# Kernel tuning notes

Hardware: AMD Instinct MI355X
Metric: run time of the kernel (lower is better)

Reference implementation:

```python
import jax, jax.numpy as jnp
import numpy as np

N_NODES = 50000
N_EDGES = 800000


def setup_inputs() -> dict:
    key = jax.random.key(0)
    ks = jax.random.split(key, 9)
    d, h, hd = 128, 4, 32
    s = 1.0 / np.sqrt(d)
    return {
        "x": jax.random.normal(ks[0], (N_NODES, d), jnp.float32),
        "edge_index": jax.random.randint(ks[1], (2, N_EDGES), 0, N_NODES, jnp.int32),
        "W0": jax.random.normal(ks[2], (d, d), jnp.float32) * s,
        "att_l0": jax.random.normal(ks[3], (h, hd), jnp.float32) * s,
        "att_r0": jax.random.normal(ks[4], (h, hd), jnp.float32) * s,
        "b0": jnp.zeros((d,), jnp.float32),
        "W1": jax.random.normal(ks[5], (d, d), jnp.float32) * s,
        "att_l1": jax.random.normal(ks[6], (h, hd), jnp.float32) * s,
        "att_r1": jax.random.normal(ks[7], (h, hd), jnp.float32) * s,
        "b1": jnp.zeros((hd,), jnp.float32),
    }


def _gat_layer(x, src, dst, W, att_l, att_r, bias, concat):
    # x: [N, F_in]; W: [H*D, F_in] (torch Linear layout); att_*: [H, D]
    n = x.shape[0]
    h, d = att_l.shape
    hx = (x @ W.T).reshape(n, h, d)                     # [N,H,D]
    al = jnp.einsum('nhd,hd->nh', hx, att_l)            # [N,H]
    ar = jnp.einsum('nhd,hd->nh', hx, att_r)
    att = al[src] + ar[dst]                             # [E,H]
    att = jax.nn.leaky_relu(att, negative_slope=0.2)
    # segment softmax over destination nodes
    m = jax.ops.segment_max(att, dst, num_segments=n)   # [N,H]
    att = jnp.exp(att - m[dst])
    ssum = jax.ops.segment_sum(att, dst, num_segments=n)
    att = att / (ssum[dst] + 1e-9)                      # [E,H]
    msgs = att[:, :, None] * hx[src]                    # [E,H,D]
    out = jax.ops.segment_sum(msgs, dst, num_segments=n)  # [N,H,D]
    if concat:
        out = out.reshape(n, h * d)
    else:
        out = out.mean(axis=1)
    return out + bias


def reference(x, edge_index, W0, att_l0, att_r0, b0, W1, att_l1, att_r1, b1):
    src, dst = edge_index[0], edge_index[1]
    x = _gat_layer(x, src, dst, W0, att_l0, att_r0, b0, concat=True)
    x = jax.nn.relu(x)  # dropout is identity in eval mode
    x = _gat_layer(x, src, dst, W1, att_l1, att_r1, b1, concat=False)
    return x
```

## Files before the change

### kernel.cpp

```cpp
#include <hip/hip_runtime.h>
#include <hip/hip_bf16.h>

#define H 4
#define D 32
#define F 128
#define MAXDEG 64
#define PF 16
#define NBUCK 256
#define BUCKW 196
#define NABLK 128
#define SEGCAP 64
#define GB    1563
#define HXP   136

typedef __attribute__((ext_vector_type(8))) short bf16x8;
typedef __attribute__((ext_vector_type(4))) float f32x4;

__device__ __forceinline__ short f2bf(float v) {
    __hip_bfloat16 h = __float2bfloat16(v);
    return *reinterpret_cast<short*>(&h);
}
__device__ __forceinline__ float bf2f(short s) {
    __hip_bfloat16 h = *reinterpret_cast<__hip_bfloat16*>(&s);
    return __bfloat162float(h);
}

__device__ __forceinline__
void wconv_part(int part8, const float* __restrict__ W0, short* __restrict__ W0hi,
                short* __restrict__ W0lo, const float* __restrict__ W1,
                short* __restrict__ W1hi, short* __restrict__ W1lo) {
    const int tid = threadIdx.x;
    const float* W  = (part8 < 4) ? W0 : W1;
    short* Whi = (part8 < 4) ? W0hi : W1hi;
    short* Wlo = (part8 < 4) ? W0lo : W1lo;
    const int part = part8 & 3;
    const int base = part * (F * F / 4);
    for (int i = base + tid * 4; i < base + F * F / 4; i += 1024) {
        float4 v = *reinterpret_cast<const float4*>(W + i);
        float vv[4] = {v.x, v.y, v.z, v.w};
        short hs[4], ls[4];
#pragma unroll
        for (int j = 0; j < 4; ++j) {
            hs[j] = f2bf(vv[j]);
            ls[j] = f2bf(vv[j] - bf2f(hs[j]));
        }
        *reinterpret_cast<short4*>(Whi + i) = make_short4(hs[0], hs[1], hs[2], hs[3]);
        *reinterpret_cast<short4*>(Wlo + i) = make_short4(ls[0], ls[1], ls[2], ls[3]);
    }
}

__device__ __forceinline__
void bucketA_body(int abid, const int* __restrict__ ei, int E,
                  int* __restrict__ cntmat, unsigned int* __restrict__ buf) {
    __shared__ int lcnt[NBUCK];
    const int tid = threadIdx.x;
    lcnt[tid] = 0;
    __syncthreads();
    const int per = ((E / NABLK) + 3) & ~3;
    const int e0 = abid * per;
    const int e1 = min(e0 + per, E);
    for (int e = e0 + 4 * tid; e < e1; e += 1024) {
        int4 dv = *reinterpret_cast<const int4*>(ei + E + e);
        atomicAdd(&lcnt[dv.x / BUCKW], 1);
        atomicAdd(&lcnt[dv.y / BUCKW], 1);
        atomicAdd(&lcnt[dv.z / BUCKW], 1);
        atomicAdd(&lcnt[dv.w / BUCKW], 1);
    }
    __syncthreads();
    cntmat[abid * NBUCK + tid] = min(lcnt[tid], SEGCAP);
    lcnt[tid] = 0;
    __syncthreads();
    for (int e = e0 + 4 * tid; e < e1; e += 1024) {
        int4 sv = *reinterpret_cast<const int4*>(ei + e);
        int4 dv = *reinterpret_cast<const int4*>(ei + E + e);
        int ss[4] = {sv.x, sv.y, sv.z, sv.w};
        int dd[4] = {dv.x, dv.y, dv.z, dv.w};
#pragma unroll
        for (int j = 0; j < 4; ++j) {
            int b = dd[j] / BUCKW;
            int pos = atomicAdd(&lcnt[b], 1);
            if (pos < SEGCAP)
                buf[((size_t)b * NABLK + abid) * SEGCAP + pos] =
                    (unsigned)ss[j] | ((unsigned)(dd[j] - b * BUCKW) << 16);
        }
    }
}

__global__ __launch_bounds__(256)
void k_init(const int* __restrict__ ei, int E, int* __restrict__ cntmat,
            unsigned int* __restrict__ buf,
            const float* __restrict__ W0, short* __restrict__ W0hi,
            short* __restrict__ W0lo, const float* __restrict__ W1,
            short* __restrict__ W1hi, short* __restrict__ W1lo) {
    const int bid = blockIdx.x;
    if (bid < NABLK)
        bucketA_body(bid, ei, E, cntmat, buf);
    else
        wconv_part(bid - NABLK, W0, W0hi, W0lo, W1, W1hi, W1lo);
}

__device__ __forceinline__
void bucketB_body(int b, const unsigned int* __restrict__ buf,
                  const int* __restrict__ cntmat, int* __restrict__ deg,
                  unsigned short* __restrict__ ssrc2u, int N,
                  int* cnt, int* scnt, unsigned short* slots) {
    const int tid = threadIdx.x;
    if (tid < BUCKW) cnt[tid] = 0;
    if (tid < NABLK) scnt[tid] = cntmat[tid * NBUCK + b];
    __syncthreads();
    const int a    = tid & (NABLK - 1);
    const int half = tid >> 7;
    const int mm   = scnt[a];
    const unsigned int* seg = buf + ((size_t)b * NABLK + a) * SEGCAP;
    for (int c = half * 4; c < mm; c += 8) {
        uint4 r = *reinterpret_cast<const uint4*>(seg + c);
        unsigned rr[4] = {r.x, r.y, r.z, r.w};
#pragma unroll
        for (int j = 0; j < 4; ++j) {
            if (c + j < mm) {
                int src  = rr[j] & 0xffff;
                int ldst = rr[j] >> 16;
                int slot = atomicAdd(&cnt[ldst], 1);
                if (slot < MAXDEG)
                    slots[ldst * MAXDEG + slot] = (unsigned short)src;
            }
        }
    }
    __syncthreads();
    uint4* dst = reinterpret_cast<uint4*>(ssrc2u + (size_t)b * BUCKW * MAXDEG);
    const uint4* s4 = reinterpret_cast<const uint4*>(slots);
    for (int i = tid; i < BUCKW * MAXDEG / 8; i += 256)
        dst[i] = s4[i];
    if (tid < BUCKW) {
        int node = b * BUCKW + tid;
        if (node < N) deg[node] = cnt[tid];
    }
}

__device__ __forceinline__
void bsetup_pre(const short* __restrict__ Whi, const short* __restrict__ Wlo,
                int wave, int m, int q8, bf16x8 Bhi[2][4], bf16x8 Blo[2][4]) {
#pragma unroll
    for (int j = 0; j < 2; ++j) {
        const int fout = wave * 32 + j * 16 + m;
#pragma unroll
        for (int kc = 0; kc < 4; ++kc) {
            Bhi[j][kc] = *reinterpret_cast<const bf16x8*>(Whi + (size_t)fout * F + kc * 32 + q8);
            Blo[j][kc] = *reinterpret_cast<const bf16x8*>(Wlo + (size_t)fout * F + kc * 32 + q8);
        }
    }
}

__device__ __forceinline__
void loadA_f32(const float* __restrict__ X, int node0, int m, int q8, float4 r[8]) {
    const float* xp = X + (size_t)(node0 + m) * F + q8;
#pragma unroll
    for (int kc = 0; kc < 4; ++kc) {
        r[2 * kc]     = *reinterpret_cast<const float4*>(xp + kc * 32);
        r[2 * kc + 1] = *reinterpret_cast<const float4*>(xp + kc * 32 + 4);
    }
}

__device__ __forceinline__
void splitA(const float4 r[8], bf16x8 Ahi[4], bf16x8 Alo[4]) {
#pragma unroll
    for (int kc = 0; kc < 4; ++kc) {
        float xv[8] = {r[2 * kc].x, r[2 * kc].y, r[2 * kc].z, r[2 * kc].w,
                       r[2 * kc + 1].x, r[2 * kc + 1].y, r[2 * kc + 1].z, r[2 * kc + 1].w};
#pragma unroll
        for (int t2 = 0; t2 < 8; ++t2) {
            short hh = f2bf(xv[t2]);
            Ahi[kc][t2] = hh;
            Alo[kc][t2] = f2bf(xv[t2] - bf2f(hh));
        }
    }
}

__device__ __forceinline__
void mfma_epi(int tile, const bf16x8 Ahi[4], const bf16x8 Alo[4],
              const bf16x8 Bhi[2][4], const bf16x8 Blo[2][4],
              float alw0, float alw16, float arw0, float arw16,
              short* hxs, float* __restrict__ AL,
              float* __restrict__ AR, int wave, int m, int q) {
    const int node0 = tile * 16;
    f32x4 acc0 = {0.f, 0.f, 0.f, 0.f};
    f32x4 acc1 = {0.f, 0.f, 0.f, 0.f};
#pragma unroll
    for (int kc = 0; kc < 4; ++kc) {
        acc0 = __builtin_amdgcn_mfma_f32_16x16x32_bf16(Ahi[kc], Bhi[0][kc], acc0, 0, 0, 0);
        acc1 = __builtin_amdgcn_mfma_f32_16x16x32_bf16(Ahi[kc], Bhi[1][kc], acc1, 0, 0, 0);
        acc0 = __builtin_amdgcn_mfma_f32_16x16x32_bf16(Ahi[kc], Blo[0][kc], acc0, 0, 0, 0);
        acc1 = __builtin_amdgcn_mfma_f32_16x16x32_bf16(Ahi[kc], Blo[1][kc], acc1, 0, 0, 0);
        acc0 = __builtin_amdgcn_mfma_f32_16x16x32_bf16(Alo[kc], Bhi[0][kc], acc0, 0, 0, 0);
        acc1 = __builtin_amdgcn_mfma_f32_16x16x32_bf16(Alo[kc], Bhi[1][kc], acc1, 0, 0, 0);
    }
    const int row0 = node0 + q * 4;
    const int col0 = wave * 32 + m;
#pragma unroll
    for (int r = 0; r < 4; ++r) {
        hxs[(q * 4 + r) * HXP + col0]      = f2bf(acc0[r]);
        hxs[(q * 4 + r) * HXP + col0 + 16] = f2bf(acc1[r]);
        float pal = acc0[r] * alw0 + acc1[r] * alw16;
        float par = acc0[r] * arw0 + acc1[r] * arw16;
#pragma unroll
        for (int o = 1; o < 16; o <<= 1) {
            pal += __shfl_xor(pal, o);
            par += __shfl_xor(par, o);
        }
        if (m == 0) {
            AL[(size_t)(row0 + r) * H + wave] = pal;
            AR[(size_t)(row0 + r) * H + wave] = par;
        }
    }
}

__device__ __forceinline__
void hxb_writeout(const short* hxs, int tile, __hip_bfloat16* __restrict__ HXB) {
    const int tid = threadIdx.x;
    const int row = tid >> 4;
    const int col = (tid & 15) * 8;
    uint4 v = *reinterpret_cast<const uint4*>(hxs + row * HXP + col);
    *reinterpret_cast<uint4*>(reinterpret_cast<short*>(HXB) +
                              (size_t)(tile * 16 + row) * F + col) = v;
}

__device__ __forceinline__
void gemm_pair_f32(int bid, const float* __restrict__ X,
                   const short* __restrict__ Whi, const short* __restrict__ Wlo,
                   const float* __restrict__ attl, const float* __restrict__ attr,
                   __hip_bfloat16* __restrict__ HXB, float* __restrict__ AL,
                   float* __restrict__ AR, int ntiles, short* hxs) {
    const int wave = threadIdx.x >> 6;
    const int lane = threadIdx.x & 63;
    const int m    = lane & 15;
    const int q    = lane >> 4;
    const int q8   = q * 8;
    bf16x8 Bhi[2][4], Blo[2][4];
    bsetup_pre(Whi, Wlo, wave, m, q8, Bhi, Blo);
    const float alw0  = attl[wave * 32 + m];
    const float alw16 = attl[wave * 32 + 16 + m];
    const float arw0  = attr[wave * 32 + m];
    const float arw16 = attr[wave * 32 + 16 + m];

    const int t0 = bid, t1 = bid + GB;
    const bool has1 = t1 < ntiles;
    float4 r0[8], r1[8];
    loadA_f32(X, t0 * 16, m, q8, r0);
    if (has1) loadA_f32(X, t1 * 16, m, q8, r1);
    bf16x8 Ahi[4], Alo[4];
    splitA(r0, Ahi, Alo);
    mfma_epi(t0, Ahi, Alo, Bhi, Blo, alw0, alw16, arw0, arw16, hxs, AL, AR, wave, m, q);
    if (has1) {
        splitA(r1, Ahi, Alo);
        mfma_epi(t1, Ahi, Alo, Bhi, Blo, alw0, alw16, arw0, arw16,
                 hxs + 16 * HXP, AL, AR, wave, m, q);
    }
    __syncthreads();
    hxb_writeout(hxs, t0, HXB);
    if (has1) hxb_writeout(hxs + 16 * HXP, t1, HXB);
}

__global__ __launch_bounds__(256)
void k_mid(const unsigned int* __restrict__ buf, const int* __restrict__ cntmat,
           int* __restrict__ deg, unsigned short* __restrict__ ssrc2u, int N,
           const float* __restrict__ X, const short* __restrict__ W0hi,
           const short* __restrict__ W0lo, const float* __restrict__ attl0,
           const float* __restrict__ attr0, __hip_bfloat16* __restrict__ HXB,
           float* __restrict__ AL, float* __restrict__ AR, int ntiles) {
    __shared__ union {
        struct {
            int cnt[BUCKW];
            int scnt[NABLK];
            unsigned short slots[BUCKW * MAXDEG];
        } bb;
        short hxs[2 * 16 * HXP];
    } sm;
    const int bid = blockIdx.x;
    if (bid < NBUCK)
        bucketB_body(bid, buf, cntmat, deg, ssrc2u, N,
                     sm.bb.cnt, sm.bb.scnt, sm.bb.slots);
    else
        gemm_pair_f32(bid - NBUCK, X, W0hi, W0lo, attl0, attr0, HXB, AL, AR,
                      ntiles, sm.hxs);
}

__device__ __forceinline__
int stage_node32(int g2, int lt, int n, const unsigned short* __restrict__ ssrc2u,
                 const int* __restrict__ deg, const float* __restrict__ AL,
                 const float4 ar4, int (*sidx)[MAXDEG], float (*sw)[MAXDEG][H]) {
    const int cnt  = min(deg[n], MAXDEG);
    const int rcnt = (cnt + PF - 1) & ~(PF - 1);
    for (int t2 = lt; t2 < rcnt; t2 += 32) {
        if (t2 < cnt) {
            int s = ssrc2u[(size_t)n * MAXDEG + t2];
            sidx[g2][t2] = s;
            float4 al4 = *reinterpret_cast<const float4*>(AL + (size_t)s * H);
            float a0 = al4.x + ar4.x; a0 = a0 > 0.f ? a0 : 0.2f * a0;
            float a1 = al4.y + ar4.y; a1 = a1 > 0.f ? a1 : 0.2f * a1;
            float a2 = al4.z + ar4.z; a2 = a2 > 0.f ? a2 : 0.2f * a2;
            float a3 = al4.w + ar4.w; a3 = a3 > 0.f ? a3 : 0.2f * a3;
            sw[g2][t2][0] = __expf(a0);
            sw[g2][t2][1] = __expf(a1);
            sw[g2][t2][2] = __expf(a2);
            sw[g2][t2][3] = __expf(a3);
        } else {
            sidx[g2][t2] = 0;
            sw[g2][t2][0] = 0.f; sw[g2][t2][1] = 0.f;
            sw[g2][t2][2] = 0.f; sw[g2][t2][3] = 0.f;
        }
    }
    __builtin_amdgcn_wave_barrier();
    return rcnt;
}

__device__ __forceinline__
void gather32(int g2, int lt, int rcnt, const __hip_bfloat16* __restrict__ HXB,
              const int (*sidx)[MAXDEG], const float (*sw)[MAXDEG][H],
              float& a0, float& a1, float& a2, float& a3, float& wsum) {
    const int h = lt >> 3;
    const unsigned short* hx = reinterpret_cast<const unsigned short*>(HXB);
    for (int base = 0; base < rcnt; base += PF) {
        ushort4 v[PF];
#pragma unroll
        for (int j = 0; j < PF; ++j) {
            int s = sidx[g2][base + j];
            v[j] = *reinterpret_cast<const ushort4*>(hx + (size_t)s * F + 4 * lt);
        }
#pragma unroll
        for (int j = 0; j < PF; ++j) {
            float w = sw[g2][base + j][h];
            a0 += w * bf2f((short)v[j].x);
            a1 += w * bf2f((short)v[j].y);
            a2 += w * bf2f((short)v[j].z);
            a3 += w * bf2f((short)v[j].w);
            wsum += w;
        }
    }
}

__global__ __launch_bounds__(256)
void k_ag1(const unsigned short* __restrict__ ssrc2u, const int* __restrict__ deg,
           const float* __restrict__ AL0, const float* __restrict__ AR0,
           const __hip_bfloat16* __restrict__ HXB0, const float* __restrict__ b0,
           const short* __restrict__ W1hi, const short* __restrict__ W1lo,
           const float* __restrict__ attl1, const float* __restrict__ attr1,
           __hip_bfloat16* __restrict__ HXB1, float* __restrict__ AL1,
           float* __restrict__ AR1, int ntiles) {
    __shared__ int   sidx[8][MAXDEG];
    __shared__ float sw[8][MAXDEG][H];
    __shared__ short x1h[16 * HXP];
    __shared__ short x1l[16 * HXP];
    const int tid  = threadIdx.x;
    const int g2   = tid >> 5;
    const int lt   = tid & 31;
    const int tile = blockIdx.x;

#pragma unroll
    for (int r = 0; r < 2; ++r) {
        const int n = tile * 16 + r * 8 + g2;
        const float4 ar4 = *reinterpret_cast<const float4*>(AR0 + (size_t)n * H);
        int rcnt = stage_node32(g2, lt, n, ssrc2u, deg, AL0, ar4, sidx, sw);
        float a0 = 0.f, a1 = 0.f, a2 = 0.f, a3 = 0.f, ws = 0.f;
        gather32(g2, lt, rcnt, HXB0, sidx, sw, a0, a1, a2, a3, ws);
        float inv = 1.f / (ws + 1e-9f);
        const float4 b4 = *reinterpret_cast<const float4*>(b0 + 4 * lt);
        float o0 = fmaxf(a0 * inv + b4.x, 0.f);
        float o1 = fmaxf(a1 * inv + b4.y, 0.f);
        float o2 = fmaxf(a2 * inv + b4.z, 0.f);
        float o3 = fmaxf(a3 * inv + b4.w, 0.f);
        short h0 = f2bf(o0), h1 = f2bf(o1), h2 = f2bf(o2), h3 = f2bf(o3);
        short l0 = f2bf(o0 - bf2f(h0)), l1 = f2bf(o1 - bf2f(h1));
        short l2 = f2bf(o2 - bf2f(h2)), l3 = f2bf(o3 - bf2f(h3));
        const int row = r * 8 + g2;
        uint2 hw, lw;
        hw.x = (unsigned)(unsigned short)h0 | ((unsigned)(unsigned short)h1 << 16);
        hw.y = (unsigned)(unsigned short)h2 | ((unsigned)(unsigned short)h3 << 16);
        lw.x = (unsigned)(unsigned short)l0 | ((unsigned)(unsigned short)l1 << 16);
        lw.y = (unsigned)(unsigned short)l2 | ((unsigned)(unsigned short)l3 << 16);
        *reinterpret_cast<uint2*>(x1h + row * HXP + 4 * lt) = hw;
        *reinterpret_cast<uint2*>(x1l + row * HXP + 4 * lt) = lw;
    }
    __syncthreads();

    short* hxs = reinterpret_cast<short*>(sw);
    {
        const int wave = tid >> 6;
        const int lane = tid & 63;
        const int m    = lane & 15;
        const int q    = lane >> 4;
        const int q8   = q * 8;
        bf16x8 Bhi[2][4], Blo[2][4];
        bsetup_pre(W1hi, W1lo, wave, m, q8, Bhi, Blo);
        const float alw0  = attl1[wave * 32 + m];
        const float alw16 = attl1[wave * 32 + 16 + m];
        const float arw0  = attr1[wave * 32 + m];
        const float arw16 = attr1[wave * 32 + 16 + m];
        bf16x8 Ahi[4], Alo[4];
#pragma unroll
        for (int kc = 0; kc < 4; ++kc) {
            Ahi[kc] = *reinterpret_cast<const bf16x8*>(x1h + m * HXP + kc * 32 + q8);
            Alo[kc] = *reinterpret_cast<const bf16x8*>(x1l + m * HXP + kc * 32 + q8);
        }
        mfma_epi(tile, Ahi, Alo, Bhi, Blo, alw0, alw16, arw0, arw16,
                 hxs, AL1, AR1, wave, m, q);
    }
    __syncthreads();
    hxb_writeout(hxs, tile, HXB1);
}

__global__ __launch_bounds__(256)
void k_aggr1(const unsigned short* __restrict__ ssrc2u, const int* __restrict__ deg,
             const float* __restrict__ AL, const float* __restrict__ AR,
             const __hip_bfloat16* __restrict__ HXB, const float* __restrict__ bias,
             float* __restrict__ out, int N) {
    __shared__ int   sidx[8][MAXDEG];
    __shared__ float sw[8][MAXDEG][H];
    const int tid = threadIdx.x;
    const int g2  = tid >> 5;
    const int lt  = tid & 31;
    const int n   = blockIdx.x * 8 + g2;
    const float4 ar4 = *reinterpret_cast<const float4*>(AR + (size_t)n * H);
    int rcnt = stage_node32(g2, lt, n, ssrc2u, deg, AL, ar4, sidx, sw);
    float a0 = 0.f, a1 = 0.f, a2 = 0.f, a3 = 0.f, ws = 0.f;
    gather32(g2, lt, rcnt, HXB, sidx, sw, a0, a1, a2, a3, ws);
    float inv = 1.f / (ws + 1e-9f);
    float v0 = a0 * inv, v1 = a1 * inv, v2 = a2 * inv, v3 = a3 * inv;
    v0 += __shfl_xor(v0, 8);  v1 += __shfl_xor(v1, 8);
    v2 += __shfl_xor(v2, 8);  v3 += __shfl_xor(v3, 8);
    v0 += __shfl_xor(v0, 16); v1 += __shfl_xor(v1, 16);
    v2 += __shfl_xor(v2, 16); v3 += __shfl_xor(v3, 16);
    if (lt < 8) {
        const float4 b4 = *reinterpret_cast<const float4*>(bias + 4 * lt);
        float4 o;
        o.x = 0.25f * v0 + b4.x;
        o.y = 0.25f * v1 + b4.y;
        o.z = 0.25f * v2 + b4.z;
        o.w = 0.25f * v3 + b4.w;
        *reinterpret_cast<float4*>(out + (size_t)n * D + 4 * lt) = o;
    }
}

extern "C" void kernel_launch(void* const* d_in, const int* in_sizes, int n_in,
                              void* d_out, int out_size, void* d_ws, size_t ws_size,
                              hipStream_t stream) {
    const float* x     = (const float*)d_in[0];
    const int*   ei    = (const int*)d_in[1];
    const float* W0    = (const float*)d_in[2];
    const float* attl0 = (const float*)d_in[3];
    const float* attr0 = (const float*)d_in[4];
    const float* b0    = (const float*)d_in[5];
    const float* W1    = (const float*)d_in[6];
    const float* attl1 = (const float*)d_in[7];
    const float* attr1 = (const float*)d_in[8];
    const float* b1    = (const float*)d_in[9];

    const int N = in_sizes[0] / F;
    const int E = in_sizes[1] / 2;
    const int ntiles = N / 16;

    char* p = (char*)d_ws;
    __hip_bfloat16* HXB0 = (__hip_bfloat16*)p; p += (size_t)N * F * 2;
    __hip_bfloat16* HXB1 = (__hip_bfloat16*)p; p += (size_t)N * F * 2;
    short* W0hi = (short*)p;                   p += (size_t)F * F * 2;
    short* W0lo = (short*)p;                   p += (size_t)F * F * 2;
    short* W1hi = (short*)p;                   p += (size_t)F * F * 2;
    short* W1lo = (short*)p;                   p += (size_t)F * F * 2;
    float* AL0  = (float*)p;                   p += (size_t)N * H * 4;
    float* AR0  = (float*)p;                   p += (size_t)N * H * 4;
    float* AL1  = (float*)p;                   p += (size_t)N * H * 4;
    float* AR1  = (float*)p;                   p += (size_t)N * H * 4;
    unsigned short* ssrc2u = (unsigned short*)p;
    p += (size_t)NBUCK * BUCKW * MAXDEG * 2;
    int* deg = (int*)p;                        p += (size_t)N * 4;
    unsigned int* buf = (unsigned int*)p;      p += (size_t)NBUCK * NABLK * SEGCAP * 4;
    int* cntmat = (int*)p;

    k_init<<<NABLK + 8, 256, 0, stream>>>(ei, E, cntmat, buf,
                                          W0, W0hi, W0lo, W1, W1hi, W1lo);

    k_mid<<<NBUCK + GB, 256, 0, stream>>>(buf, cntmat, deg, ssrc2u, N,
                                          x, W0hi, W0lo, attl0, attr0,
                                          HXB0, AL0, AR0, ntiles);

    k_ag1<<<ntiles, 256, 0, stream>>>(ssrc2u, deg, AL0, AR0, HXB0, b0,
                                      W1hi, W1lo, attl1, attr1,
                                      HXB1, AL1, AR1, ntiles);

    k_aggr1<<<N / 8, 256, 0, stream>>>(ssrc2u, deg, AL1, AR1, HXB1, b1,
                                       (float*)d_out, N);
}
```

Baseline: 214.8 us.

## Drop init kernel: full-scan bucketing per block and in-register W0 split

Removes the separate k_init launch and its two-pass bucket staging buffer. Each of the 256 bucket blocks now scans the full destination array and keeps only the edges whose destination falls in its range. The W0 hi/lo bf16 split is computed in registers inside each GEMM block, and the W1 conversion moves into four extra blocks of k_mid. This saves a launch and global round-trips, but every bucket block now reads all 800K destinations, so total reads grow about 256-fold and each block's runtime likely lengthens.

```diff
diff --git a/kernel.cpp b/kernel.cpp
--- a/kernel.cpp
+++ b/kernel.cpp
@@ -8,8 +8,6 @@
 #define PF 16
 #define NBUCK 256
 #define BUCKW 196
-#define NABLK 128
-#define SEGCAP 64
 #define GB    1563
 #define HXP   136
 
@@ -26,17 +24,12 @@
 }
 
 __device__ __forceinline__
-void wconv_part(int part8, const float* __restrict__ W0, short* __restrict__ W0hi,
-                short* __restrict__ W0lo, const float* __restrict__ W1,
-                short* __restrict__ W1hi, short* __restrict__ W1lo) {
+void wconv_part(int part, const float* __restrict__ W1, short* __restrict__ W1hi,
+                short* __restrict__ W1lo) {
     const int tid = threadIdx.x;
-    const float* W  = (part8 < 4) ? W0 : W1;
-    short* Whi = (part8 < 4) ? W0hi : W1hi;
-    short* Wlo = (part8 < 4) ? W0lo : W1lo;
-    const int part = part8 & 3;
     const int base = part * (F * F / 4);
     for (int i = base + tid * 4; i < base + F * F / 4; i += 1024) {
-        float4 v = *reinterpret_cast<const float4*>(W + i);
+        float4 v = *reinterpret_cast<const float4*>(W1 + i);
         float vv[4] = {v.x, v.y, v.z, v.w};
         short hs[4], ls[4];
 #pragma unroll
@@ -44,85 +37,30 @@
             hs[j] = f2bf(vv[j]);
             ls[j] = f2bf(vv[j] - bf2f(hs[j]));
         }
-        *reinterpret_cast<short4*>(Whi + i) = make_short4(hs[0], hs[1], hs[2], hs[3]);
-        *reinterpret_cast<short4*>(Wlo + i) = make_short4(ls[0], ls[1], ls[2], ls[3]);
-    }
-}
-
-__device__ __forceinline__
-void bucketA_body(int abid, const int* __restrict__ ei, int E,
-                  int* __restrict__ cntmat, unsigned int* __restrict__ buf) {
-    __shared__ int lcnt[NBUCK];
-    const int tid = threadIdx.x;
-    lcnt[tid] = 0;
-    __syncthreads();
-    const int per = ((E / NABLK) + 3) & ~3;
-    const int e0 = abid * per;
-    const int e1 = min(e0 + per, E);
-    for (int e = e0 + 4 * tid; e < e1; e += 1024) {
-        int4 dv = *reinterpret_cast<const int4*>(ei + E + e);
-        atomicAdd(&lcnt[dv.x / BUCKW], 1);
-        atomicAdd(&lcnt[dv.y / BUCKW], 1);
-        atomicAdd(&lcnt[dv.z / BUCKW], 1);
-        atomicAdd(&lcnt[dv.w / BUCKW], 1);
-    }
-    __syncthreads();
-    cntmat[abid * NBUCK + tid] = min(lcnt[tid], SEGCAP);
-    lcnt[tid] = 0;
-    __syncthreads();
-    for (int e = e0 + 4 * tid; e < e1; e += 1024) {
-        int4 sv = *reinterpret_cast<const int4*>(ei + e);
-        int4 dv = *reinterpret_cast<const int4*>(ei + E + e);
-        int ss[4] = {sv.x, sv.y, sv.z, sv.w};
-        int dd[4] = {dv.x, dv.y, dv.z, dv.w};
-#pragma unroll
-        for (int j = 0; j < 4; ++j) {
-            int b = dd[j] / BUCKW;
-            int pos = atomicAdd(&lcnt[b], 1);
-            if (pos < SEGCAP)
-                buf[((size_t)b * NABLK + abid) * SEGCAP + pos] =
-                    (unsigned)ss[j] | ((unsigned)(dd[j] - b * BUCKW) << 16);
-        }
-    }
-}
-
-__global__ __launch_bounds__(256)
-void k_init(const int* __restrict__ ei, int E, int* __restrict__ cntmat,
-            unsigned int* __restrict__ buf,
-            const float* __restrict__ W0, short* __restrict__ W0hi,
-            short* __restrict__ W0lo, const float* __restrict__ W1,
-            short* __restrict__ W1hi, short* __restrict__ W1lo) {
-    const int bid = blockIdx.x;
-    if (bid < NABLK)
-        bucketA_body(bid, ei, E, cntmat, buf);
-    else
-        wconv_part(bid - NABLK, W0, W0hi, W0lo, W1, W1hi, W1lo);
-}
-
-__device__ __forceinline__
-void bucketB_body(int b, const unsigned int* __restrict__ buf,
-                  const int* __restrict__ cntmat, int* __restrict__ deg,
-                  unsigned short* __restrict__ ssrc2u, int N,
-                  int* cnt, int* scnt, unsigned short* slots) {
+        *reinterpret_cast<short4*>(W1hi + i) = make_short4(hs[0], hs[1], hs[2], hs[3]);
+        *reinterpret_cast<short4*>(W1lo + i) = make_short4(ls[0], ls[1], ls[2], ls[3]);
+    }
+}
+
+__device__ __forceinline__
+void bucket_scan_body(int b, const int* __restrict__ ei, int E,
+                      int* __restrict__ deg, unsigned short* __restrict__ ssrc2u,
+                      int N, int* cnt, unsigned short* slots) {
     const int tid = threadIdx.x;
     if (tid < BUCKW) cnt[tid] = 0;
-    if (tid < NABLK) scnt[tid] = cntmat[tid * NBUCK + b];
     __syncthreads();
-    const int a    = tid & (NABLK - 1);
-    const int half = tid >> 7;
-    const int mm   = scnt[a];
-    const unsigned int* seg = buf + ((size_t)b * NABLK + a) * SEGCAP;
-    for (int c = half * 4; c < mm; c += 8) {
-        uint4 r = *reinterpret_cast<const uint4*>(seg + c);
-        unsigned rr[4] = {r.x, r.y, r.z, r.w};
+    const int lo = b * BUCKW, hi = lo + BUCKW;
+    for (int e = 4 * tid; e < E; e += 1024) {
+        int4 dv = *reinterpret_cast<const int4*>(ei + E + e);
+        int dd[4] = {dv.x, dv.y, dv.z, dv.w};
 #pragma unroll
         for (int j = 0; j < 4; ++j) {
-            if (c + j < mm) {
-                int src  = rr[j] & 0xffff;
-                int ldst = rr[j] >> 16;
-                int slot = atomicAdd(&cnt[ldst], 1);
+            int d = dd[j];
+            if (d >= lo && d < hi) {
+                int src  = ei[e + j];
+                int slot = atomicAdd(&cnt[d - lo], 1);
                 if (slot < MAXDEG)
-                    slots[ldst * MAXDEG + slot] = (unsigned short)src;
+                    slots[(d - lo) * MAXDEG + slot] = (unsigned short)src;
             }
         }
     }
@@ -138,6 +76,28 @@
 }
 
 __device__ __forceinline__
+void bsetup_fp32(const float* __restrict__ W, int wave, int m, int q8,
+                 bf16x8 Bhi[2][4], bf16x8 Blo[2][4]) {
+#pragma unroll
+    for (int j = 0; j < 2; ++j) {
+        const int fout = wave * 32 + j * 16 + m;
+#pragma unroll
+        for (int kc = 0; kc < 4; ++kc) {
+            const float* wp = W + (size_t)fout * F + kc * 32 + q8;
+            float4 w0 = *reinterpret_cast<const float4*>(wp);
+            float4 w1 = *reinterpret_cast<const float4*>(wp + 4);
+            float wv[8] = {w0.x, w0.y, w0.z, w0.w, w1.x, w1.y, w1.z, w1.w};
+#pragma unroll
+            for (int t2 = 0; t2 < 8; ++t2) {
+                short hh = f2bf(wv[t2]);
+                Bhi[j][kc][t2] = hh;
+                Blo[j][kc][t2] = f2bf(wv[t2] - bf2f(hh));
+            }
+        }
+    }
+}
+
+__device__ __forceinline__
 void bsetup_pre(const short* __restrict__ Whi, const short* __restrict__ Wlo,
                 int wave, int m, int q8, bf16x8 Bhi[2][4], bf16x8 Blo[2][4]) {
 #pragma unroll
@@ -226,7 +186,7 @@
 
 __device__ __forceinline__
 void gemm_pair_f32(int bid, const float* __restrict__ X,
-                   const short* __restrict__ Whi, const short* __restrict__ Wlo,
+                   const float* __restrict__ W0,
                    const float* __restrict__ attl, const float* __restrict__ attr,
                    __hip_bfloat16* __restrict__ HXB, float* __restrict__ AL,
                    float* __restrict__ AR, int ntiles, short* hxs) {
@@ -235,18 +195,17 @@
     const int m    = lane & 15;
     const int q    = lane >> 4;
     const int q8   = q * 8;
-    bf16x8 Bhi[2][4], Blo[2][4];
-    bsetup_pre(Whi, Wlo, wave, m, q8, Bhi, Blo);
-    const float alw0  = attl[wave * 32 + m];
-    const float alw16 = attl[wave * 32 + 16 + m];
-    const float arw0  = attr[wave * 32 + m];
-    const float arw16 = attr[wave * 32 + 16 + m];
-
     const int t0 = bid, t1 = bid + GB;
     const bool has1 = t1 < ntiles;
     float4 r0[8], r1[8];
     loadA_f32(X, t0 * 16, m, q8, r0);
     if (has1) loadA_f32(X, t1 * 16, m, q8, r1);
+    bf16x8 Bhi[2][4], Blo[2][4];
+    bsetup_fp32(W0, wave, m, q8, Bhi, Blo);
+    const float alw0  = attl[wave * 32 + m];
+    const float alw16 = attl[wave * 32 + 16 + m];
+    const float arw0  = attr[wave * 32 + m];
+    const float arw16 = attr[wave * 32 + 16 + m];
     bf16x8 Ahi[4], Alo[4];
     splitA(r0, Ahi, Alo);
     mfma_epi(t0, Ahi, Alo, Bhi, Blo, alw0, alw16, arw0, arw16, hxs, AL, AR, wave, m, q);
@@ -261,26 +220,28 @@
 }
 
 __global__ __launch_bounds__(256)
-void k_mid(const unsigned int* __restrict__ buf, const int* __restrict__ cntmat,
-           int* __restrict__ deg, unsigned short* __restrict__ ssrc2u, int N,
-           const float* __restrict__ X, const short* __restrict__ W0hi,
-           const short* __restrict__ W0lo, const float* __restrict__ attl0,
-           const float* __restrict__ attr0, __hip_bfloat16* __restrict__ HXB,
-           float* __restrict__ AL, float* __restrict__ AR, int ntiles) {
+void k_mid(const int* __restrict__ ei, int E, int* __restrict__ deg,
+           unsigned short* __restrict__ ssrc2u, int N,
+           const float* __restrict__ X, const float* __restrict__ W0,
+           const float* __restrict__ attl0, const float* __restrict__ attr0,
+           __hip_bfloat16* __restrict__ HXB, float* __restrict__ AL,
+           float* __restrict__ AR, int ntiles,
+           const float* __restrict__ W1, short* __restrict__ W1hi,
+           short* __restrict__ W1lo) {
     __shared__ union {
         struct {
             int cnt[BUCKW];
-            int scnt[NABLK];
             unsigned short slots[BUCKW * MAXDEG];
         } bb;
         short hxs[2 * 16 * HXP];
     } sm;
     const int bid = blockIdx.x;
     if (bid < NBUCK)
-        bucketB_body(bid, buf, cntmat, deg, ssrc2u, N,
-                     sm.bb.cnt, sm.bb.scnt, sm.bb.slots);
+        bucket_scan_body(bid, ei, E, deg, ssrc2u, N, sm.bb.cnt, sm.bb.slots);
+    else if (bid < NBUCK + 4)
+        wconv_part(bid - NBUCK, W1, W1hi, W1lo);
     else
-        gemm_pair_f32(bid - NBUCK, X, W0hi, W0lo, attl0, attr0, HXB, AL, AR,
+        gemm_pair_f32(bid - NBUCK - 4, X, W0, attl0, attr0, HXB, AL, AR,
                       ntiles, sm.hxs);
 }
 
@@ -461,8 +422,6 @@
     char* p = (char*)d_ws;
     __hip_bfloat16* HXB0 = (__hip_bfloat16*)p; p += (size_t)N * F * 2;
     __hip_bfloat16* HXB1 = (__hip_bfloat16*)p; p += (size_t)N * F * 2;
-    short* W0hi = (short*)p;                   p += (size_t)F * F * 2;
-    short* W0lo = (short*)p;                   p += (size_t)F * F * 2;
     short* W1hi = (short*)p;                   p += (size_t)F * F * 2;
     short* W1lo = (short*)p;                   p += (size_t)F * F * 2;
     float* AL0  = (float*)p;                   p += (size_t)N * H * 4;
@@ -471,16 +430,12 @@
     float* AR1  = (float*)p;                   p += (size_t)N * H * 4;
     unsigned short* ssrc2u = (unsigned short*)p;
     p += (size_t)NBUCK * BUCKW * MAXDEG * 2;
-    int* deg = (int*)p;                        p += (size_t)N * 4;
-    unsigned int* buf = (unsigned int*)p;      p += (size_t)NBUCK * NABLK * SEGCAP * 4;
-    int* cntmat = (int*)p;
-
-    k_init<<<NABLK + 8, 256, 0, stream>>>(ei, E, cntmat, buf,
-                                          W0, W0hi, W0lo, W1, W1hi, W1lo);
-
-    k_mid<<<NBUCK + GB, 256, 0, stream>>>(buf, cntmat, deg, ssrc2u, N,
-                                          x, W0hi, W0lo, attl0, attr0,
-                                          HXB0, AL0, AR0, ntiles);
+    int* deg = (int*)p;
+
+    k_mid<<<NBUCK + 4 + GB, 256, 0, stream>>>(ei, E, deg, ssrc2u, N,
+                                              x, W0, attl0, attr0,
+                                              HXB0, AL0, AR0, ntiles,
+                                              W1, W1hi, W1lo);
 
     k_ag1<<<ntiles, 256, 0, stream>>>(ssrc2u, deg, AL0, AR0, HXB0, b0,
                                       W1hi, W1lo, attl1, attr1,
```

Result: slower. 520.3 us (+142.2%).

## Use 16 lanes per node with 16-byte gathers in GAT aggregation kernels

Applied to the files above, without the earlier changes.

Changes the aggregation mapping from 32 lanes per node (8-byte bf16x4 loads) to 16 lanes per node (16-byte loads of 8 bf16), so each block handles 16 nodes at once and k_ag1 no longer loops over two rows. PF drops from 16 to 8, which keeps register use in check but pads degree to a multiple of 8 rather than 16. The aim is wider memory transactions and more nodes in flight per block. The cost is more edge iterations per lane, so fewer lanes share each neighbour list, and the staging loop now covers edges with 16 lanes.

```diff
diff --git a/kernel.cpp b/kernel.cpp
--- a/kernel.cpp
+++ b/kernel.cpp
@@ -5,7 +5,7 @@
 #define D 32
 #define F 128
 #define MAXDEG 64
-#define PF 16
+#define PF 8
 #define NBUCK 256
 #define BUCKW 196
 #define NABLK 128
@@ -285,28 +285,28 @@
 }
 
 __device__ __forceinline__
-int stage_node32(int g2, int lt, int n, const unsigned short* __restrict__ ssrc2u,
+int stage_node16(int g, int lt, int n, const unsigned short* __restrict__ ssrc2u,
                  const int* __restrict__ deg, const float* __restrict__ AL,
                  const float4 ar4, int (*sidx)[MAXDEG], float (*sw)[MAXDEG][H]) {
     const int cnt  = min(deg[n], MAXDEG);
     const int rcnt = (cnt + PF - 1) & ~(PF - 1);
-    for (int t2 = lt; t2 < rcnt; t2 += 32) {
+    for (int t2 = lt; t2 < rcnt; t2 += 16) {
         if (t2 < cnt) {
             int s = ssrc2u[(size_t)n * MAXDEG + t2];
-            sidx[g2][t2] = s;
+            sidx[g][t2] = s;
             float4 al4 = *reinterpret_cast<const float4*>(AL + (size_t)s * H);
             float a0 = al4.x + ar4.x; a0 = a0 > 0.f ? a0 : 0.2f * a0;
             float a1 = al4.y + ar4.y; a1 = a1 > 0.f ? a1 : 0.2f * a1;
             float a2 = al4.z + ar4.z; a2 = a2 > 0.f ? a2 : 0.2f * a2;
             float a3 = al4.w + ar4.w; a3 = a3 > 0.f ? a3 : 0.2f * a3;
-            sw[g2][t2][0] = __expf(a0);
-            sw[g2][t2][1] = __expf(a1);
-            sw[g2][t2][2] = __expf(a2);
-            sw[g2][t2][3] = __expf(a3);
+            sw[g][t2][0] = __expf(a0);
+            sw[g][t2][1] = __expf(a1);
+            sw[g][t2][2] = __expf(a2);
+            sw[g][t2][3] = __expf(a3);
         } else {
-            sidx[g2][t2] = 0;
-            sw[g2][t2][0] = 0.f; sw[g2][t2][1] = 0.f;
-            sw[g2][t2][2] = 0.f; sw[g2][t2][3] = 0.f;
+            sidx[g][t2] = 0;
+            sw[g][t2][0] = 0.f; sw[g][t2][1] = 0.f;
+            sw[g][t2][2] = 0.f; sw[g][t2][3] = 0.f;
         }
     }
     __builtin_amdgcn_wave_barrier();
@@ -314,25 +314,27 @@
 }
 
 __device__ __forceinline__
-void gather32(int g2, int lt, int rcnt, const __hip_bfloat16* __restrict__ HXB,
+void gather16(int g, int lt, int rcnt, const __hip_bfloat16* __restrict__ HXB,
               const int (*sidx)[MAXDEG], const float (*sw)[MAXDEG][H],
-              float& a0, float& a1, float& a2, float& a3, float& wsum) {
-    const int h = lt >> 3;
+              float a[8], float& wsum) {
+    const int h = lt >> 2;
     const unsigned short* hx = reinterpret_cast<const unsigned short*>(HXB);
     for (int base = 0; base < rcnt; base += PF) {
-        ushort4 v[PF];
+        uint4 v[PF];
 #pragma unroll
         for (int j = 0; j < PF; ++j) {
-            int s = sidx[g2][base + j];
-            v[j] = *reinterpret_cast<const ushort4*>(hx + (size_t)s * F + 4 * lt);
+            int s = sidx[g][base + j];
+            v[j] = *reinterpret_cast<const uint4*>(hx + (size_t)s * F + 8 * lt);
         }
 #pragma unroll
         for (int j = 0; j < PF; ++j) {
-            float w = sw[g2][base + j][h];
-            a0 += w * bf2f((short)v[j].x);
-            a1 += w * bf2f((short)v[j].y);
-            a2 += w * bf2f((short)v[j].z);
-            a3 += w * bf2f((short)v[j].w);
+            float w = sw[g][base + j][h];
+            unsigned ww[4] = {v[j].x, v[j].y, v[j].z, v[j].w};
+#pragma unroll
+            for (int k = 0; k < 4; ++k) {
+                a[2 * k]     += w * bf2f((short)(ww[k] & 0xffff));
+                a[2 * k + 1] += w * bf2f((short)(ww[k] >> 16));
+            }
             wsum += w;
         }
     }
@@ -346,39 +348,40 @@
            const float* __restrict__ attl1, const float* __restrict__ attr1,
            __hip_bfloat16* __restrict__ HXB1, float* __restrict__ AL1,
            float* __restrict__ AR1, int ntiles) {
-    __shared__ int   sidx[8][MAXDEG];
-    __shared__ float sw[8][MAXDEG][H];
+    __shared__ int   sidx[16][MAXDEG];
+    __shared__ float sw[16][MAXDEG][H];
     __shared__ short x1h[16 * HXP];
     __shared__ short x1l[16 * HXP];
     const int tid  = threadIdx.x;
-    const int g2   = tid >> 5;
-    const int lt   = tid & 31;
+    const int g    = tid >> 4;
+    const int lt   = tid & 15;
     const int tile = blockIdx.x;
 
-#pragma unroll
-    for (int r = 0; r < 2; ++r) {
-        const int n = tile * 16 + r * 8 + g2;
+    {
+        const int n = tile * 16 + g;
         const float4 ar4 = *reinterpret_cast<const float4*>(AR0 + (size_t)n * H);
-        int rcnt = stage_node32(g2, lt, n, ssrc2u, deg, AL0, ar4, sidx, sw);
-        float a0 = 0.f, a1 = 0.f, a2 = 0.f, a3 = 0.f, ws = 0.f;
-        gather32(g2, lt, rcnt, HXB0, sidx, sw, a0, a1, a2, a3, ws);
+        int rcnt = stage_node16(g, lt, n, ssrc2u, deg, AL0, ar4, sidx, sw);
+        float a[8] = {0.f, 0.f, 0.f, 0.f, 0.f, 0.f, 0.f, 0.f};
+        float ws = 0.f;
+        gather16(g, lt, rcnt, HXB0, sidx, sw, a, ws);
         float inv = 1.f / (ws + 1e-9f);
-        const float4 b4 = *reinterpret_cast<const float4*>(b0 + 4 * lt);
-        float o0 = fmaxf(a0 * inv + b4.x, 0.f);
-        float o1 = fmaxf(a1 * inv + b4.y, 0.f);
-        float o2 = fmaxf(a2 * inv + b4.z, 0.f);
-        float o3 = fmaxf(a3 * inv + b4.w, 0.f);
-        short h0 = f2bf(o0), h1 = f2bf(o1), h2 = f2bf(o2), h3 = f2bf(o3);
-        short l0 = f2bf(o0 - bf2f(h0)), l1 = f2bf(o1 - bf2f(h1));
-        short l2 = f2bf(o2 - bf2f(h2)), l3 = f2bf(o3 - bf2f(h3));
-        const int row = r * 8 + g2;
-        uint2 hw, lw;
-        hw.x = (unsigned)(unsigned short)h0 | ((unsigned)(unsigned short)h1 << 16);
-        hw.y = (unsigned)(unsigned short)h2 | ((unsigned)(unsigned short)h3 << 16);
-        lw.x = (unsigned)(unsigned short)l0 | ((unsigned)(unsigned short)l1 << 16);
-        lw.y = (unsigned)(unsigned short)l2 | ((unsigned)(unsigned short)l3 << 16);
-        *reinterpret_cast<uint2*>(x1h + row * HXP + 4 * lt) = hw;
-        *reinterpret_cast<uint2*>(x1l + row * HXP + 4 * lt) = lw;
+        const float4 b4a = *reinterpret_cast<const float4*>(b0 + 8 * lt);
+        const float4 b4b = *reinterpret_cast<const float4*>(b0 + 8 * lt + 4);
+        float bb[8] = {b4a.x, b4a.y, b4a.z, b4a.w, b4b.x, b4b.y, b4b.z, b4b.w};
+        unsigned hw[4], lw[4];
+#pragma unroll
+        for (int k = 0; k < 4; ++k) {
+            float o0 = fmaxf(a[2 * k] * inv + bb[2 * k], 0.f);
+            float o1 = fmaxf(a[2 * k + 1] * inv + bb[2 * k + 1], 0.f);
+            short h0 = f2bf(o0), h1 = f2bf(o1);
+            short l0 = f2bf(o0 - bf2f(h0)), l1 = f2bf(o1 - bf2f(h1));
+            hw[k] = (unsigned)(unsigned short)h0 | ((unsigned)(unsigned short)h1 << 16);
+            lw[k] = (unsigned)(unsigned short)l0 | ((unsigned)(unsigned short)l1 << 16);
+        }
+        uint4 hv = {hw[0], hw[1], hw[2], hw[3]};
+        uint4 lv = {lw[0], lw[1], lw[2], lw[3]};
+        *reinterpret_cast<uint4*>(x1h + g * HXP + 8 * lt) = hv;
+        *reinterpret_cast<uint4*>(x1l + g * HXP + 8 * lt) = lv;
     }
     __syncthreads();
 
@@ -413,30 +416,39 @@
              const float* __restrict__ AL, const float* __restrict__ AR,
              const __hip_bfloat16* __restrict__ HXB, const float* __restrict__ bias,
              float* __restrict__ out, int N) {
-    __shared__ int   sidx[8][MAXDEG];
-    __shared__ float sw[8][MAXDEG][H];
+    __shared__ int   sidx[16][MAXDEG];
+    __shared__ float sw[16][MAXDEG][H];
     const int tid = threadIdx.x;
-    const int g2  = tid >> 5;
-    const int lt  = tid & 31;
-    const int n   = blockIdx.x * 8 + g2;
+    const int g   = tid >> 4;
+    const int lt  = tid & 15;
+    const int n   = blockIdx.x * 16 + g;
     const float4 ar4 = *reinterpret_cast<const float4*>(AR + (size_t)n * H);
-    int rcnt = stage_node32(g2, lt, n, ssrc2u, deg, AL, ar4, sidx, sw);
-    float a0 = 0.f, a1 = 0.f, a2 = 0.f, a3 = 0.f, ws = 0.f;
-    gather32(g2, lt, rcnt, HXB, sidx, sw, a0, a1, a2, a3, ws);
+    int rcnt = stage_node16(g, lt, n, ssrc2u, deg, AL, ar4, sidx, sw);
+    float a[8] = {0.f, 0.f, 0.f, 0.f, 0.f, 0.f, 0.f, 0.f};
+    float ws = 0.f;
+    gather16(g, lt, rcnt, HXB, sidx, sw, a, ws);
     float inv = 1.f / (ws + 1e-9f);
-    float v0 = a0 * inv, v1 = a1 * inv, v2 = a2 * inv, v3 = a3 * inv;
-    v0 += __shfl_xor(v0, 8);  v1 += __shfl_xor(v1, 8);
-    v2 += __shfl_xor(v2, 8);  v3 += __shfl_xor(v3, 8);
-    v0 += __shfl_xor(v0, 16); v1 += __shfl_xor(v1, 16);
-    v2 += __shfl_xor(v2, 16); v3 += __shfl_xor(v3, 16);
-    if (lt < 8) {
-        const float4 b4 = *reinterpret_cast<const float4*>(bias + 4 * lt);
-        float4 o;
-        o.x = 0.25f * v0 + b4.x;
-        o.y = 0.25f * v1 + b4.y;
-        o.z = 0.25f * v2 + b4.z;
-        o.w = 0.25f * v3 + b4.w;
-        *reinterpret_cast<float4*>(out + (size_t)n * D + 4 * lt) = o;
+    float v[8];
+#pragma unroll
+    for (int k = 0; k < 8; ++k) {
+        v[k] = a[k] * inv;
+        v[k] += __shfl_xor(v[k], 4);
+        v[k] += __shfl_xor(v[k], 8);
+    }
+    if (lt < 4) {
+        const float4 b4a = *reinterpret_cast<const float4*>(bias + 8 * lt);
+        const float4 b4b = *reinterpret_cast<const float4*>(bias + 8 * lt + 4);
+        float4 o0, o1;
+        o0.x = 0.25f * v[0] + b4a.x;
+        o0.y = 0.25f * v[1] + b4a.y;
+        o0.z = 0.25f * v[2] + b4a.z;
+        o0.w = 0.25f * v[3] + b4a.w;
+        o1.x = 0.25f * v[4] + b4b.x;
+        o1.y = 0.25f * v[5] + b4b.y;
+        o1.z = 0.25f * v[6] + b4b.z;
+        o1.w = 0.25f * v[7] + b4b.w;
+        *reinterpret_cast<float4*>(out + (size_t)n * D + 8 * lt)     = o0;
+        *reinterpret_cast<float4*>(out + (size_t)n * D + 8 * lt + 4) = o1;
     }
 }
 
@@ -486,6 +498,6 @@
                                       W1hi, W1lo, attl1, attr1,
                                       HXB1, AL1, AR1, ntiles);
 
-    k_aggr1<<<N / 8, 256, 0, stream>>>(ssrc2u, deg, AL1, AR1, HXB1, b1,
-                                       (float*)d_out, N);
-}
+    k_aggr1<<<ntiles, 256, 0, stream>>>(ssrc2u, deg, AL1, AR1, HXB1, b1,
+                                        (float*)d_out, N);
+}
```

New measurement: 210.4 us. -2.1%, faster.
